# Kernel optimization log

Hardware: AMD Instinct MI355X
Metric: run time of the kernel (lower is better)

The kernel has to match this reference:

```python
import jax, jax.numpy as jnp
import numpy as np

B, T, E, H = 8, 1024, 128, 8
S = E // H  # 16, narrow per-head dim


def setup_inputs() -> dict:
    key = jax.random.key(0)
    ks = jax.random.split(key, 7)
    return {
        "x": jax.random.normal(ks[0], (B, T, E), dtype=jnp.float32),
        "masks": jax.random.randint(ks[1], (B, T), 0, 2, dtype=jnp.int32),
        "Wq": jax.random.normal(ks[2], (S, S), dtype=jnp.float32) * 0.05,
        "Wk": jax.random.normal(ks[3], (S, S), dtype=jnp.float32) * 0.05,
        "Wv": jax.random.normal(ks[4], (S, S), dtype=jnp.float32) * 0.05,
        "Wu": jax.random.normal(ks[5], (E, E), dtype=jnp.float32) * 0.05,
        "bu": jnp.zeros((E,), dtype=jnp.float32),
        "temporal_only": 1,
    }


def reference(x, masks, Wq, Wk, Wv, Wu, bu, temporal_only):
    b, t, e = x.shape
    h = H
    s = e // h
    x4 = x.reshape(b, t, h, s)
    # nn.Linear(s, s, bias=False): y = x @ W.T, applied per head
    q = jnp.einsum('bths,ds->bthd', x4, Wq)
    k = jnp.einsum('bths,ds->bthd', x4, Wk)
    v = jnp.einsum('bths,ds->bthd', x4, Wv)
    scale = jnp.float32(e) ** 0.25
    q = q / scale
    k = k / scale
    # (b, h, t, t) attention logits
    dot = jnp.einsum('bqhd,bkhd->bhqk', q, k)
    # temporal_only masking: masks is (b, t), applied on key axis then query axis
    m = masks.astype(bool)
    neg = jnp.float32(-1e9)
    dot = jnp.where(m[:, None, None, :], dot, neg)
    dot = jnp.where(m[:, None, :, None], dot, neg)
    attn = jax.nn.softmax(dot, axis=-1)
    # post-softmax zeroing with the same masks
    attn = jnp.where(m[:, None, None, :], attn, jnp.float32(0.0))
    attn = jnp.where(m[:, None, :, None], attn, jnp.float32(0.0))
    out = jnp.einsum('bhqk,bkhd->bqhd', attn, v).reshape(b, t, h * s)
    return out @ Wu.T + bu
```

## Files before the change

### kernel.cpp

```cpp
#include <hip/hip_runtime.h>

#define NB 8
#define NT 1024
#define NE 128
#define NH 8
#define NS 16

#define WS_Q 0
#define WS_K 1048576
#define WS_V 2097152
#define WS_Y 3145728
#define WS_VIDX 4194304

#define WT_PITCH 132

static __device__ __forceinline__ void fma4(float4& acc, float s, const float4 v) {
  acc.x = fmaf(s, v.x, acc.x);
  acc.y = fmaf(s, v.y, acc.y);
  acc.z = fmaf(s, v.z, acc.z);
  acc.w = fmaf(s, v.w, acc.w);
}

static __device__ __forceinline__ float dot16(const float4 x0, const float4 x1,
                                              const float4 x2, const float4 x3,
                                              const float4 w0, const float4 w1,
                                              const float4 w2, const float4 w3) {
  float s0 = (x0.x * w0.x + x0.y * w0.y) + (x0.z * w0.z + x0.w * w0.w);
  float s1 = (x1.x * w1.x + x1.y * w1.y) + (x1.z * w1.z + x1.w * w1.w);
  float s2 = (x2.x * w2.x + x2.y * w2.y) + (x2.z * w2.z + x2.w * w2.w);
  float s3 = (x3.x * w3.x + x3.y * w3.y) + (x3.z * w3.z + x3.w * w3.w);
  return (s0 + s1) + (s2 + s3);
}

__global__ __launch_bounds__(256) void qkv_kernel(
    const float* __restrict__ x, const int* __restrict__ masks,
    const float* __restrict__ Wq, const float* __restrict__ Wk,
    const float* __restrict__ Wv, float* __restrict__ Q, float* __restrict__ K,
    float* __restrict__ V, int* __restrict__ vidx, int* __restrict__ vcount) {
  if (blockIdx.x >= 1024) {
    const int b = blockIdx.x - 1024;
    const int lane = threadIdx.x;
    if (lane < 64) {
      int base = 0;
      for (int c = 0; c < NT; c += 64) {
        int t = c + lane;
        int v = masks[b * NT + t] != 0;
        unsigned long long bal = __ballot(v);
        int pos = base + __popcll(bal & ((1ull << lane) - 1ull));
        if (v) vidx[b * NT + pos] = t;
        base += __popcll(bal);
      }
      if (lane == 0) vcount[b] = base;
    }
    return;
  }
  const int tid = threadIdx.x;
  const int h = blockIdx.x & 7;
  const int rg = blockIdx.x >> 3;
  const int b = rg >> 4;
  const int base = rg << 6;
  const int d = tid & 15;
  const int r = base + ((tid >> 4) << 2);
  const float4* wq4 = (const float4*)(Wq + d * 16);
  const float4 wq0 = wq4[0], wq1 = wq4[1], wq2 = wq4[2], wq3 = wq4[3];
  const float4* wk4 = (const float4*)(Wk + d * 16);
  const float4 wk0 = wk4[0], wk1 = wk4[1], wk2 = wk4[2], wk3 = wk4[3];
  const float4* wv4 = (const float4*)(Wv + d * 16);
  const float4 wv0 = wv4[0], wv1 = wv4[1], wv2 = wv4[2], wv3 = wv4[3];
  const float invs = 0.08838834764831845f;
#pragma unroll
  for (int i = 0; i < 4; i++) {
    const int row = r + i;
    const float4* xp = (const float4*)(x + (size_t)row * 128 + h * 16);
    const float4 x0 = xp[0], x1 = xp[1], x2 = xp[2], x3 = xp[3];
    float aq = dot16(x0, x1, x2, x3, wq0, wq1, wq2, wq3);
    float ak = dot16(x0, x1, x2, x3, wk0, wk1, wk2, wk3);
    float av = dot16(x0, x1, x2, x3, wv0, wv1, wv2, wv3);
    const int t = row & 1023;
    size_t o = ((size_t)(b * NH + h) * NT + t) * NS + d;
    Q[o] = aq * invs;
    K[o] = ak;
    V[o] = av;
  }
}

__global__ __launch_bounds__(256) void attn_kernel(
    const float* __restrict__ Q, const float* __restrict__ K,
    const float* __restrict__ V, const int* __restrict__ masks,
    const int* __restrict__ vidx, const int* __restrict__ vcount,
    float* __restrict__ Y) {
  __shared__ __align__(16) float Ks[2048];
  __shared__ __align__(16) float Vs[2048];
  __shared__ __align__(16) float om[2][4][64][20];
  __shared__ float ml[2][4][64][2];
  const int tid = threadIdx.x;
  const int lane = tid & 63;
  const int split = tid >> 6;
  const int bh = blockIdx.x >> 3;
  const int b = bh >> 3, h = bh & 7;
  const int tbase = (blockIdx.x & 7) << 7;
  const int tA = tbase + lane;
  const int nv = vcount[b];
  const float4* qga = (const float4*)(Q + ((size_t)bh * NT + tA) * NS);
  const float4 qa0 = qga[0], qa1 = qga[1], qa2 = qga[2], qa3 = qga[3];
  const float4* qgb = (const float4*)(Q + ((size_t)bh * NT + tA + 64) * NS);
  const float4 qb0 = qgb[0], qb1 = qgb[1], qb2 = qgb[2], qb3 = qgb[3];
  float mA = -1e30f, lA = 0.f, mB = -1e30f, lB = 0.f;
  float4 oa0 = {0, 0, 0, 0}, oa1 = {0, 0, 0, 0}, oa2 = {0, 0, 0, 0},
         oa3 = {0, 0, 0, 0};
  float4 ob0 = {0, 0, 0, 0}, ob1 = {0, 0, 0, 0}, ob2 = {0, 0, 0, 0},
         ob3 = {0, 0, 0, 0};

  for (int k0 = 0; k0 < nv; k0 += 128) {
    __syncthreads();
    const int quad = tid & 3;
    const int jr = tid >> 2;
#pragma unroll
    for (int p = 0; p < 2; p++) {
      int row = jr + (p << 6);
      int j = k0 + row;
      float4 kv = {0, 0, 0, 0}, vv = {0, 0, 0, 0};
      if (j < nv) {
        int kk = vidx[b * NT + j];
        size_t bse = ((size_t)bh * NT + kk) * NS + (quad << 2);
        kv = *(const float4*)(K + bse);
        vv = *(const float4*)(V + bse);
      }
      *(float4*)(Ks + row * 16 + (quad << 2)) = kv;
      *(float4*)(Vs + row * 16 + (quad << 2)) = vv;
    }
    __syncthreads();
    int jmax = nv - k0;
    if (jmax > 128) jmax = 128;
    for (int g = 0; g < 8; g++) {
      const int rbase = split + (g << 4);
      if (rbase >= jmax) break;
      float sA[4], sB[4];
#pragma unroll
      for (int i = 0; i < 4; i++) {
        const float4* kr = (const float4*)(Ks + (rbase + (i << 2)) * 16);
        float4 k0v = kr[0], k1v = kr[1], k2v = kr[2], k3v = kr[3];
        sA[i] = dot16(qa0, qa1, qa2, qa3, k0v, k1v, k2v, k3v);
        sB[i] = dot16(qb0, qb1, qb2, qb3, k0v, k1v, k2v, k3v);
      }
#pragma unroll
      for (int i = 0; i < 4; i++)
        if (rbase + (i << 2) >= jmax) { sA[i] = -1e30f; sB[i] = -1e30f; }
      float mbA = fmaxf(fmaxf(sA[0], sA[1]), fmaxf(sA[2], sA[3]));
      if (mbA > mA) {
        float al = __expf(mA - mbA);
        lA *= al;
        oa0.x *= al; oa0.y *= al; oa0.z *= al; oa0.w *= al;
        oa1.x *= al; oa1.y *= al; oa1.z *= al; oa1.w *= al;
        oa2.x *= al; oa2.y *= al; oa2.z *= al; oa2.w *= al;
        oa3.x *= al; oa3.y *= al; oa3.z *= al; oa3.w *= al;
        mA = mbA;
      }
      float pA[4];
      pA[0] = __expf(sA[0] - mA); pA[1] = __expf(sA[1] - mA);
      pA[2] = __expf(sA[2] - mA); pA[3] = __expf(sA[3] - mA);
      lA += (pA[0] + pA[1]) + (pA[2] + pA[3]);
      float mbB = fmaxf(fmaxf(sB[0], sB[1]), fmaxf(sB[2], sB[3]));
      if (mbB > mB) {
        float al = __expf(mB - mbB);
        lB *= al;
        ob0.x *= al; ob0.y *= al; ob0.z *= al; ob0.w *= al;
        ob1.x *= al; ob1.y *= al; ob1.z *= al; ob1.w *= al;
        ob2.x *= al; ob2.y *= al; ob2.z *= al; ob2.w *= al;
        ob3.x *= al; ob3.y *= al; ob3.z *= al; ob3.w *= al;
        mB = mbB;
      }
      float pB[4];
      pB[0] = __expf(sB[0] - mB); pB[1] = __expf(sB[1] - mB);
      pB[2] = __expf(sB[2] - mB); pB[3] = __expf(sB[3] - mB);
      lB += (pB[0] + pB[1]) + (pB[2] + pB[3]);
#pragma unroll
      for (int i = 0; i < 4; i++) {
        const float4* vr = (const float4*)(Vs + (rbase + (i << 2)) * 16);
        float4 v0 = vr[0], v1 = vr[1], v2 = vr[2], v3 = vr[3];
        fma4(oa0, pA[i], v0); fma4(oa1, pA[i], v1);
        fma4(oa2, pA[i], v2); fma4(oa3, pA[i], v3);
        fma4(ob0, pB[i], v0); fma4(ob1, pB[i], v1);
        fma4(ob2, pB[i], v2); fma4(ob3, pB[i], v3);
      }
    }
  }
  ml[0][split][lane][0] = mA; ml[0][split][lane][1] = lA;
  ml[1][split][lane][0] = mB; ml[1][split][lane][1] = lB;
  {
    float* pa = &om[0][split][lane][0];
    *(float4*)(pa + 0) = oa0; *(float4*)(pa + 4) = oa1;
    *(float4*)(pa + 8) = oa2; *(float4*)(pa + 12) = oa3;
    float* pb = &om[1][split][lane][0];
    *(float4*)(pb + 0) = ob0; *(float4*)(pb + 4) = ob1;
    *(float4*)(pb + 8) = ob2; *(float4*)(pb + 12) = ob3;
  }
  __syncthreads();
  if (split < 2) {
    const int qg = split;
    const int tq = tbase + (qg << 6) + lane;
    float m0 = ml[qg][0][lane][0], l0 = ml[qg][0][lane][1];
    float m1 = ml[qg][1][lane][0], l1 = ml[qg][1][lane][1];
    float m2 = ml[qg][2][lane][0], l2 = ml[qg][2][lane][1];
    float m3 = ml[qg][3][lane][0], l3 = ml[qg][3][lane][1];
    float M = fmaxf(fmaxf(m0, m1), fmaxf(m2, m3));
    float f0 = __expf(m0 - M), f1 = __expf(m1 - M), f2 = __expf(m2 - M),
          f3 = __expf(m3 - M);
    float L = f0 * l0 + f1 * l1 + f2 * l2 + f3 * l3;
    float4 y0 = {0, 0, 0, 0}, y1 = {0, 0, 0, 0}, y2 = {0, 0, 0, 0},
           y3 = {0, 0, 0, 0};
    float fs[4] = {f0, f1, f2, f3};
#pragma unroll
    for (int s = 0; s < 4; s++) {
      const float* p = &om[qg][s][lane][0];
      fma4(y0, fs[s], *(const float4*)(p + 0));
      fma4(y1, fs[s], *(const float4*)(p + 4));
      fma4(y2, fs[s], *(const float4*)(p + 8));
      fma4(y3, fs[s], *(const float4*)(p + 12));
    }
    const int qm = masks[b * NT + tq];
    const float inv = (qm != 0 && L > 0.f) ? (1.0f / L) : 0.f;
    y0.x *= inv; y0.y *= inv; y0.z *= inv; y0.w *= inv;
    y1.x *= inv; y1.y *= inv; y1.z *= inv; y1.w *= inv;
    y2.x *= inv; y2.y *= inv; y2.z *= inv; y2.w *= inv;
    y3.x *= inv; y3.y *= inv; y3.z *= inv; y3.w *= inv;
    float4* yo = (float4*)(Y + ((size_t)b * NT + tq) * NE + h * NS);
    yo[0] = y0; yo[1] = y1; yo[2] = y2; yo[3] = y3;
  }
}

__global__ __launch_bounds__(256) void proj_kernel(
    const float* __restrict__ Y, const float* __restrict__ Wu,
    const float* __restrict__ bu, float* __restrict__ out) {
  __shared__ __align__(16) float Wt[64 * WT_PITCH];
  __shared__ __align__(16) float Yt[16 * 128];
  const int tid = threadIdx.x;
  const int r0 = blockIdx.x * 16;
  const float4* yg = (const float4*)(Y + (size_t)r0 * 128);
  float4* yt4 = (float4*)Yt;
  yt4[tid] = yg[tid];
  yt4[tid + 256] = yg[tid + 256];
  const int c0 = (tid & 31) << 2;
  const int rg = (tid >> 5) & 3;
  const int eh = tid >> 7;
  float4 acc0 = {0, 0, 0, 0}, acc1 = {0, 0, 0, 0}, acc2 = {0, 0, 0, 0},
         acc3 = {0, 0, 0, 0};
  for (int e0 = 0; e0 < 128; e0 += 64) {
    __syncthreads();
#pragma unroll
    for (int p = 0; p < 8; p++) {
      int idx = tid + p * 256;
      int c = idx >> 4;
      int es = (idx & 15) << 2;
      float4 w = *(const float4*)(Wu + c * 128 + e0 + es);
      Wt[(es + 0) * WT_PITCH + c] = w.x;
      Wt[(es + 1) * WT_PITCH + c] = w.y;
      Wt[(es + 2) * WT_PITCH + c] = w.z;
      Wt[(es + 3) * WT_PITCH + c] = w.w;
    }
    __syncthreads();
    const int eb = eh << 5;
    const float* y0 = Yt + (rg * 4 + 0) * 128 + e0 + eb;
    const float* y1 = Yt + (rg * 4 + 1) * 128 + e0 + eb;
    const float* y2 = Yt + (rg * 4 + 2) * 128 + e0 + eb;
    const float* y3 = Yt + (rg * 4 + 3) * 128 + e0 + eb;
#pragma unroll 4
    for (int e = 0; e < 32; e += 4) {
      const float* wb = Wt + (eb + e) * WT_PITCH + c0;
      float4 w0 = *(const float4*)(wb + 0 * WT_PITCH);
      float4 w1 = *(const float4*)(wb + 1 * WT_PITCH);
      float4 w2 = *(const float4*)(wb + 2 * WT_PITCH);
      float4 w3 = *(const float4*)(wb + 3 * WT_PITCH);
      float4 ya = *(const float4*)(y0 + e);
      float4 yb = *(const float4*)(y1 + e);
      float4 yc = *(const float4*)(y2 + e);
      float4 yd = *(const float4*)(y3 + e);
      fma4(acc0, ya.x, w0); fma4(acc0, ya.y, w1); fma4(acc0, ya.z, w2); fma4(acc0, ya.w, w3);
      fma4(acc1, yb.x, w0); fma4(acc1, yb.y, w1); fma4(acc1, yb.z, w2); fma4(acc1, yb.w, w3);
      fma4(acc2, yc.x, w0); fma4(acc2, yc.y, w1); fma4(acc2, yc.z, w2); fma4(acc2, yc.w, w3);
      fma4(acc3, yd.x, w0); fma4(acc3, yd.y, w1); fma4(acc3, yd.z, w2); fma4(acc3, yd.w, w3);
    }
  }
  __syncthreads();
  if (eh == 1) {
    float* p = Wt + (tid & 127) * 20;
    *(float4*)(p + 0) = acc0; *(float4*)(p + 4) = acc1;
    *(float4*)(p + 8) = acc2; *(float4*)(p + 12) = acc3;
  }
  __syncthreads();
  if (eh == 0) {
    const float* p = Wt + tid * 20;
    float4 b4 = *(const float4*)(bu + c0);
    float4 q0 = *(const float4*)(p + 0);
    float4 q1 = *(const float4*)(p + 4);
    float4 q2 = *(const float4*)(p + 8);
    float4 q3 = *(const float4*)(p + 12);
    acc0.x += q0.x + b4.x; acc0.y += q0.y + b4.y; acc0.z += q0.z + b4.z; acc0.w += q0.w + b4.w;
    acc1.x += q1.x + b4.x; acc1.y += q1.y + b4.y; acc1.z += q1.z + b4.z; acc1.w += q1.w + b4.w;
    acc2.x += q2.x + b4.x; acc2.y += q2.y + b4.y; acc2.z += q2.z + b4.z; acc2.w += q2.w + b4.w;
    acc3.x += q3.x + b4.x; acc3.y += q3.y + b4.y; acc3.z += q3.z + b4.z; acc3.w += q3.w + b4.w;
    *(float4*)(out + (size_t)(r0 + rg * 4 + 0) * 128 + c0) = acc0;
    *(float4*)(out + (size_t)(r0 + rg * 4 + 1) * 128 + c0) = acc1;
    *(float4*)(out + (size_t)(r0 + rg * 4 + 2) * 128 + c0) = acc2;
    *(float4*)(out + (size_t)(r0 + rg * 4 + 3) * 128 + c0) = acc3;
  }
}

extern "C" void kernel_launch(void* const* d_in, const int* in_sizes, int n_in,
                              void* d_out, int out_size, void* d_ws,
                              size_t ws_size, hipStream_t stream) {
  const float* x = (const float*)d_in[0];
  const int* masks = (const int*)d_in[1];
  const float* Wq = (const float*)d_in[2];
  const float* Wk = (const float*)d_in[3];
  const float* Wv = (const float*)d_in[4];
  const float* Wu = (const float*)d_in[5];
  const float* bu = (const float*)d_in[6];
  float* out = (float*)d_out;

  float* ws = (float*)d_ws;
  float* Q = ws + WS_Q;
  float* K = ws + WS_K;
  float* V = ws + WS_V;
  float* Y = ws + WS_Y;
  int* vidx = (int*)(ws + WS_VIDX);
  int* vcount = vidx + NB * NT;

  qkv_kernel<<<1024 + NB, 256, 0, stream>>>(x, masks, Wq, Wk, Wv, Q, K, V,
                                            vidx, vcount);
  attn_kernel<<<NB * NH * (NT / 128), 256, 0, stream>>>(Q, K, V, masks, vidx,
                                                        vcount, Y);
  proj_kernel<<<NB * NT / 16, 256, 0, stream>>>(Y, Wu, bu, out);
}
```

Baseline: 140.6 us.

## Restructure attention so each lane handles four queries with 16-way key split

Each block now covers 64 queries instead of 128, which doubles the grid. Each lane holds 4 query rows, so every K/V row read from LDS is reused four times. Keys are split 16 ways within the block (4 lane groups per wave across 4 waves). Partial softmax states are merged first with cross-lane shuffles and then through shared memory. This cuts LDS read traffic per FLOP and adds parallelism, at the cost of higher register pressure (64 accumulator floats plus 64 query floats) and an extra shuffle reduction stage.

```diff
diff --git a/kernel.cpp b/kernel.cpp
--- a/kernel.cpp
+++ b/kernel.cpp
@@ -19,6 +19,19 @@
   acc.y = fmaf(s, v.y, acc.y);
   acc.z = fmaf(s, v.z, acc.z);
   acc.w = fmaf(s, v.w, acc.w);
+}
+
+static __device__ __forceinline__ float dot16f(const float4 q0, const float4 q1,
+                                               const float4 q2, const float4 q3,
+                                               const float4 k0, const float4 k1,
+                                               const float4 k2, const float4 k3) {
+  float s = q0.x * k0.x;
+  s = fmaf(q0.y, k0.y, s); s = fmaf(q0.z, k0.z, s); s = fmaf(q0.w, k0.w, s);
+  s = fmaf(q1.x, k1.x, s); s = fmaf(q1.y, k1.y, s); s = fmaf(q1.z, k1.z, s);
+  s = fmaf(q1.w, k1.w, s); s = fmaf(q2.x, k2.x, s); s = fmaf(q2.y, k2.y, s);
+  s = fmaf(q2.z, k2.z, s); s = fmaf(q2.w, k2.w, s); s = fmaf(q3.x, k3.x, s);
+  s = fmaf(q3.y, k3.y, s); s = fmaf(q3.z, k3.z, s); s = fmaf(q3.w, k3.w, s);
+  return s;
 }
 
 static __device__ __forceinline__ float dot16(const float4 x0, const float4 x1,
@@ -30,6 +43,15 @@
   float s2 = (x2.x * w2.x + x2.y * w2.y) + (x2.z * w2.z + x2.w * w2.w);
   float s3 = (x3.x * w3.x + x3.y * w3.y) + (x3.z * w3.z + x3.w * w3.w);
   return (s0 + s1) + (s2 + s3);
+}
+
+static __device__ __forceinline__ float4 shfl_xor4(const float4 v, int mask) {
+  float4 r;
+  r.x = __shfl_xor(v.x, mask, 64);
+  r.y = __shfl_xor(v.y, mask, 64);
+  r.z = __shfl_xor(v.z, mask, 64);
+  r.w = __shfl_xor(v.w, mask, 64);
+  return r;
 }
 
 __global__ __launch_bounds__(256) void qkv_kernel(
@@ -91,25 +113,33 @@
     float* __restrict__ Y) {
   __shared__ __align__(16) float Ks[2048];
   __shared__ __align__(16) float Vs[2048];
-  __shared__ __align__(16) float om[2][4][64][20];
-  __shared__ float ml[2][4][64][2];
+  __shared__ __align__(16) float om[4][16][4][20];
+  __shared__ float mlw[4][16][4][2];
   const int tid = threadIdx.x;
+  const int wave = tid >> 6;
   const int lane = tid & 63;
-  const int split = tid >> 6;
-  const int bh = blockIdx.x >> 3;
+  const int grp = lane >> 4;
+  const int slot = lane & 15;
+  const int sp = (wave << 2) | grp;
+  const int bh = blockIdx.x >> 4;
   const int b = bh >> 3, h = bh & 7;
-  const int tbase = (blockIdx.x & 7) << 7;
-  const int tA = tbase + lane;
+  const int tbase = (blockIdx.x & 15) << 6;
+  const int tq = tbase + (slot << 2);
   const int nv = vcount[b];
-  const float4* qga = (const float4*)(Q + ((size_t)bh * NT + tA) * NS);
-  const float4 qa0 = qga[0], qa1 = qga[1], qa2 = qga[2], qa3 = qga[3];
-  const float4* qgb = (const float4*)(Q + ((size_t)bh * NT + tA + 64) * NS);
-  const float4 qb0 = qgb[0], qb1 = qgb[1], qb2 = qgb[2], qb3 = qgb[3];
-  float mA = -1e30f, lA = 0.f, mB = -1e30f, lB = 0.f;
-  float4 oa0 = {0, 0, 0, 0}, oa1 = {0, 0, 0, 0}, oa2 = {0, 0, 0, 0},
-         oa3 = {0, 0, 0, 0};
-  float4 ob0 = {0, 0, 0, 0}, ob1 = {0, 0, 0, 0}, ob2 = {0, 0, 0, 0},
-         ob3 = {0, 0, 0, 0};
+  const float4* qg = (const float4*)(Q + ((size_t)bh * NT + tq) * NS);
+  float4 qr[4][4];
+#pragma unroll
+  for (int i = 0; i < 4; i++) {
+#pragma unroll
+    for (int c = 0; c < 4; c++) qr[i][c] = qg[i * 4 + c];
+  }
+  float m[4] = {-1e30f, -1e30f, -1e30f, -1e30f};
+  float l[4] = {0.f, 0.f, 0.f, 0.f};
+  float4 o[4][4];
+#pragma unroll
+  for (int i = 0; i < 4; i++)
+#pragma unroll
+    for (int c = 0; c < 4; c++) o[i][c] = make_float4(0.f, 0.f, 0.f, 0.f);
 
   for (int k0 = 0; k0 < nv; k0 += 128) {
     __syncthreads();
@@ -132,99 +162,134 @@
     __syncthreads();
     int jmax = nv - k0;
     if (jmax > 128) jmax = 128;
-    for (int g = 0; g < 8; g++) {
-      const int rbase = split + (g << 4);
-      if (rbase >= jmax) break;
-      float sA[4], sB[4];
+#pragma unroll
+    for (int g = 0; g < 2; g++) {
+      const int rb = sp + (g << 6);
+      float s[4][4];
 #pragma unroll
       for (int i = 0; i < 4; i++) {
-        const float4* kr = (const float4*)(Ks + (rbase + (i << 2)) * 16);
-        float4 k0v = kr[0], k1v = kr[1], k2v = kr[2], k3v = kr[3];
-        sA[i] = dot16(qa0, qa1, qa2, qa3, k0v, k1v, k2v, k3v);
-        sB[i] = dot16(qb0, qb1, qb2, qb3, k0v, k1v, k2v, k3v);
-      }
-#pragma unroll
-      for (int i = 0; i < 4; i++)
-        if (rbase + (i << 2) >= jmax) { sA[i] = -1e30f; sB[i] = -1e30f; }
-      float mbA = fmaxf(fmaxf(sA[0], sA[1]), fmaxf(sA[2], sA[3]));
-      if (mbA > mA) {
-        float al = __expf(mA - mbA);
-        lA *= al;
-        oa0.x *= al; oa0.y *= al; oa0.z *= al; oa0.w *= al;
-        oa1.x *= al; oa1.y *= al; oa1.z *= al; oa1.w *= al;
-        oa2.x *= al; oa2.y *= al; oa2.z *= al; oa2.w *= al;
-        oa3.x *= al; oa3.y *= al; oa3.z *= al; oa3.w *= al;
-        mA = mbA;
-      }
-      float pA[4];
-      pA[0] = __expf(sA[0] - mA); pA[1] = __expf(sA[1] - mA);
-      pA[2] = __expf(sA[2] - mA); pA[3] = __expf(sA[3] - mA);
-      lA += (pA[0] + pA[1]) + (pA[2] + pA[3]);
-      float mbB = fmaxf(fmaxf(sB[0], sB[1]), fmaxf(sB[2], sB[3]));
-      if (mbB > mB) {
-        float al = __expf(mB - mbB);
-        lB *= al;
-        ob0.x *= al; ob0.y *= al; ob0.z *= al; ob0.w *= al;
-        ob1.x *= al; ob1.y *= al; ob1.z *= al; ob1.w *= al;
-        ob2.x *= al; ob2.y *= al; ob2.z *= al; ob2.w *= al;
-        ob3.x *= al; ob3.y *= al; ob3.z *= al; ob3.w *= al;
-        mB = mbB;
-      }
-      float pB[4];
-      pB[0] = __expf(sB[0] - mB); pB[1] = __expf(sB[1] - mB);
-      pB[2] = __expf(sB[2] - mB); pB[3] = __expf(sB[3] - mB);
-      lB += (pB[0] + pB[1]) + (pB[2] + pB[3]);
+        const float4* kr = (const float4*)(Ks + (rb + (i << 4)) * 16);
+        const float4 k0v = kr[0], k1v = kr[1], k2v = kr[2], k3v = kr[3];
+#pragma unroll
+        for (int q = 0; q < 4; q++)
+          s[i][q] = dot16f(qr[q][0], qr[q][1], qr[q][2], qr[q][3], k0v, k1v,
+                           k2v, k3v);
+      }
 #pragma unroll
       for (int i = 0; i < 4; i++) {
-        const float4* vr = (const float4*)(Vs + (rbase + (i << 2)) * 16);
-        float4 v0 = vr[0], v1 = vr[1], v2 = vr[2], v3 = vr[3];
-        fma4(oa0, pA[i], v0); fma4(oa1, pA[i], v1);
-        fma4(oa2, pA[i], v2); fma4(oa3, pA[i], v3);
-        fma4(ob0, pB[i], v0); fma4(ob1, pB[i], v1);
-        fma4(ob2, pB[i], v2); fma4(ob3, pB[i], v3);
-      }
-    }
-  }
-  ml[0][split][lane][0] = mA; ml[0][split][lane][1] = lA;
-  ml[1][split][lane][0] = mB; ml[1][split][lane][1] = lB;
-  {
-    float* pa = &om[0][split][lane][0];
-    *(float4*)(pa + 0) = oa0; *(float4*)(pa + 4) = oa1;
-    *(float4*)(pa + 8) = oa2; *(float4*)(pa + 12) = oa3;
-    float* pb = &om[1][split][lane][0];
-    *(float4*)(pb + 0) = ob0; *(float4*)(pb + 4) = ob1;
-    *(float4*)(pb + 8) = ob2; *(float4*)(pb + 12) = ob3;
+        if (rb + (i << 4) >= jmax) {
+          s[i][0] = -1e30f; s[i][1] = -1e30f; s[i][2] = -1e30f; s[i][3] = -1e30f;
+        }
+      }
+      float p[4][4];
+#pragma unroll
+      for (int q = 0; q < 4; q++) {
+        float mb = fmaxf(fmaxf(s[0][q], s[1][q]), fmaxf(s[2][q], s[3][q]));
+        if (mb > m[q]) {
+          float al = __expf(m[q] - mb);
+          l[q] *= al;
+#pragma unroll
+          for (int c = 0; c < 4; c++) {
+            o[q][c].x *= al; o[q][c].y *= al; o[q][c].z *= al; o[q][c].w *= al;
+          }
+          m[q] = mb;
+        }
+        p[0][q] = __expf(s[0][q] - m[q]);
+        p[1][q] = __expf(s[1][q] - m[q]);
+        p[2][q] = __expf(s[2][q] - m[q]);
+        p[3][q] = __expf(s[3][q] - m[q]);
+        l[q] += (p[0][q] + p[1][q]) + (p[2][q] + p[3][q]);
+      }
+#pragma unroll
+      for (int i = 0; i < 4; i++) {
+        const float4* vr = (const float4*)(Vs + (rb + (i << 4)) * 16);
+        const float4 v0 = vr[0], v1 = vr[1], v2 = vr[2], v3 = vr[3];
+#pragma unroll
+        for (int q = 0; q < 4; q++) {
+          fma4(o[q][0], p[i][q], v0);
+          fma4(o[q][1], p[i][q], v1);
+          fma4(o[q][2], p[i][q], v2);
+          fma4(o[q][3], p[i][q], v3);
+        }
+      }
+    }
+  }
+#pragma unroll
+  for (int round = 0; round < 2; round++) {
+    const int xm = 16 << round;
+#pragma unroll
+    for (int q = 0; q < 4; q++) {
+      float mo = __shfl_xor(m[q], xm, 64);
+      float lo = __shfl_xor(l[q], xm, 64);
+      float4 oo0 = shfl_xor4(o[q][0], xm);
+      float4 oo1 = shfl_xor4(o[q][1], xm);
+      float4 oo2 = shfl_xor4(o[q][2], xm);
+      float4 oo3 = shfl_xor4(o[q][3], xm);
+      float M2 = fmaxf(m[q], mo);
+      float fs = __expf(m[q] - M2);
+      float fo = __expf(mo - M2);
+      l[q] = fmaf(fs, l[q], fo * lo);
+      o[q][0].x = fmaf(fs, o[q][0].x, fo * oo0.x);
+      o[q][0].y = fmaf(fs, o[q][0].y, fo * oo0.y);
+      o[q][0].z = fmaf(fs, o[q][0].z, fo * oo0.z);
+      o[q][0].w = fmaf(fs, o[q][0].w, fo * oo0.w);
+      o[q][1].x = fmaf(fs, o[q][1].x, fo * oo1.x);
+      o[q][1].y = fmaf(fs, o[q][1].y, fo * oo1.y);
+      o[q][1].z = fmaf(fs, o[q][1].z, fo * oo1.z);
+      o[q][1].w = fmaf(fs, o[q][1].w, fo * oo1.w);
+      o[q][2].x = fmaf(fs, o[q][2].x, fo * oo2.x);
+      o[q][2].y = fmaf(fs, o[q][2].y, fo * oo2.y);
+      o[q][2].z = fmaf(fs, o[q][2].z, fo * oo2.z);
+      o[q][2].w = fmaf(fs, o[q][2].w, fo * oo2.w);
+      o[q][3].x = fmaf(fs, o[q][3].x, fo * oo3.x);
+      o[q][3].y = fmaf(fs, o[q][3].y, fo * oo3.y);
+      o[q][3].z = fmaf(fs, o[q][3].z, fo * oo3.z);
+      o[q][3].w = fmaf(fs, o[q][3].w, fo * oo3.w);
+      m[q] = M2;
+    }
+  }
+  if (grp == 0) {
+#pragma unroll
+    for (int q = 0; q < 4; q++) {
+      float* pp = &om[wave][slot][q][0];
+      *(float4*)(pp + 0) = o[q][0];
+      *(float4*)(pp + 4) = o[q][1];
+      *(float4*)(pp + 8) = o[q][2];
+      *(float4*)(pp + 12) = o[q][3];
+      mlw[wave][slot][q][0] = m[q];
+      mlw[wave][slot][q][1] = l[q];
+    }
   }
   __syncthreads();
-  if (split < 2) {
-    const int qg = split;
-    const int tq = tbase + (qg << 6) + lane;
-    float m0 = ml[qg][0][lane][0], l0 = ml[qg][0][lane][1];
-    float m1 = ml[qg][1][lane][0], l1 = ml[qg][1][lane][1];
-    float m2 = ml[qg][2][lane][0], l2 = ml[qg][2][lane][1];
-    float m3 = ml[qg][3][lane][0], l3 = ml[qg][3][lane][1];
-    float M = fmaxf(fmaxf(m0, m1), fmaxf(m2, m3));
-    float f0 = __expf(m0 - M), f1 = __expf(m1 - M), f2 = __expf(m2 - M),
-          f3 = __expf(m3 - M);
-    float L = f0 * l0 + f1 * l1 + f2 * l2 + f3 * l3;
+  if (wave == 0) {
+    const int fslot = lane >> 2, fq = lane & 3;
+    float mw0 = mlw[0][fslot][fq][0], lw0 = mlw[0][fslot][fq][1];
+    float mw1 = mlw[1][fslot][fq][0], lw1 = mlw[1][fslot][fq][1];
+    float mw2 = mlw[2][fslot][fq][0], lw2 = mlw[2][fslot][fq][1];
+    float mw3 = mlw[3][fslot][fq][0], lw3 = mlw[3][fslot][fq][1];
+    float M = fmaxf(fmaxf(mw0, mw1), fmaxf(mw2, mw3));
+    float f0 = __expf(mw0 - M), f1 = __expf(mw1 - M), f2 = __expf(mw2 - M),
+          f3 = __expf(mw3 - M);
+    float L = f0 * lw0 + f1 * lw1 + f2 * lw2 + f3 * lw3;
+    float fs[4] = {f0, f1, f2, f3};
     float4 y0 = {0, 0, 0, 0}, y1 = {0, 0, 0, 0}, y2 = {0, 0, 0, 0},
            y3 = {0, 0, 0, 0};
-    float fs[4] = {f0, f1, f2, f3};
-#pragma unroll
-    for (int s = 0; s < 4; s++) {
-      const float* p = &om[qg][s][lane][0];
-      fma4(y0, fs[s], *(const float4*)(p + 0));
-      fma4(y1, fs[s], *(const float4*)(p + 4));
-      fma4(y2, fs[s], *(const float4*)(p + 8));
-      fma4(y3, fs[s], *(const float4*)(p + 12));
-    }
-    const int qm = masks[b * NT + tq];
+#pragma unroll
+    for (int w = 0; w < 4; w++) {
+      const float* pp = &om[w][fslot][fq][0];
+      fma4(y0, fs[w], *(const float4*)(pp + 0));
+      fma4(y1, fs[w], *(const float4*)(pp + 4));
+      fma4(y2, fs[w], *(const float4*)(pp + 8));
+      fma4(y3, fs[w], *(const float4*)(pp + 12));
+    }
+    const int tqq = tbase + (fslot << 2) + fq;
+    const int qm = masks[b * NT + tqq];
     const float inv = (qm != 0 && L > 0.f) ? (1.0f / L) : 0.f;
     y0.x *= inv; y0.y *= inv; y0.z *= inv; y0.w *= inv;
     y1.x *= inv; y1.y *= inv; y1.z *= inv; y1.w *= inv;
     y2.x *= inv; y2.y *= inv; y2.z *= inv; y2.w *= inv;
     y3.x *= inv; y3.y *= inv; y3.z *= inv; y3.w *= inv;
-    float4* yo = (float4*)(Y + ((size_t)b * NT + tq) * NE + h * NS);
+    float4* yo = (float4*)(Y + ((size_t)b * NT + tqq) * NE + h * NS);
     yo[0] = y0; yo[1] = y1; yo[2] = y2; yo[3] = y3;
   }
 }
@@ -328,7 +393,7 @@
 
   qkv_kernel<<<1024 + NB, 256, 0, stream>>>(x, masks, Wq, Wk, Wv, Q, K, V,
                                             vidx, vcount);
-  attn_kernel<<<NB * NH * (NT / 128), 256, 0, stream>>>(Q, K, V, masks, vidx,
-                                                        vcount, Y);
+  attn_kernel<<<NB * NH * (NT / 64), 256, 0, stream>>>(Q, K, V, masks, vidx,
+                                                       vcount, Y);
   proj_kernel<<<NB * NT / 16, 256, 0, stream>>>(Y, Wu, bu, out);
 }
```

Measured after the change: 195.2 us. +38.8%, slower.

## Split attention into 64-query blocks with 8-way key split and shuffle merge

Applied to the files above, without the earlier changes.

Each attention block now handles 64 queries instead of 128, so twice as many blocks launch. Within a block the keys are split eight ways (four waves times two half-waves). Each half-wave holds 32 queries times 2. The two half-wave partial softmax states are merged with cross-lane shuffles before the shared-memory merge across waves. The per-tile loop is fully unrolled with masking in place of an early break, and the QK dot uses a serial fma chain. This adds parallelism to fill more CUs, but each block loads K/V tiles for fewer queries, so K/V reuse drops and tile-load traffic rises.

```diff
diff --git a/kernel.cpp b/kernel.cpp
--- a/kernel.cpp
+++ b/kernel.cpp
@@ -19,6 +19,19 @@
   acc.y = fmaf(s, v.y, acc.y);
   acc.z = fmaf(s, v.z, acc.z);
   acc.w = fmaf(s, v.w, acc.w);
+}
+
+static __device__ __forceinline__ float dot16f(const float4 q0, const float4 q1,
+                                               const float4 q2, const float4 q3,
+                                               const float4 k0, const float4 k1,
+                                               const float4 k2, const float4 k3) {
+  float s = q0.x * k0.x;
+  s = fmaf(q0.y, k0.y, s); s = fmaf(q0.z, k0.z, s); s = fmaf(q0.w, k0.w, s);
+  s = fmaf(q1.x, k1.x, s); s = fmaf(q1.y, k1.y, s); s = fmaf(q1.z, k1.z, s);
+  s = fmaf(q1.w, k1.w, s); s = fmaf(q2.x, k2.x, s); s = fmaf(q2.y, k2.y, s);
+  s = fmaf(q2.z, k2.z, s); s = fmaf(q2.w, k2.w, s); s = fmaf(q3.x, k3.x, s);
+  s = fmaf(q3.y, k3.y, s); s = fmaf(q3.z, k3.z, s); s = fmaf(q3.w, k3.w, s);
+  return s;
 }
 
 static __device__ __forceinline__ float dot16(const float4 x0, const float4 x1,
@@ -91,19 +104,21 @@
     float* __restrict__ Y) {
   __shared__ __align__(16) float Ks[2048];
   __shared__ __align__(16) float Vs[2048];
-  __shared__ __align__(16) float om[2][4][64][20];
-  __shared__ float ml[2][4][64][2];
+  __shared__ __align__(16) float om[4][32][2][20];
+  __shared__ float mlw[4][32][2][2];
   const int tid = threadIdx.x;
+  const int wave = tid >> 6;
   const int lane = tid & 63;
-  const int split = tid >> 6;
-  const int bh = blockIdx.x >> 3;
+  const int slot = lane & 31;
+  const int sp = (wave << 1) | (lane >> 5);
+  const int bh = blockIdx.x >> 4;
   const int b = bh >> 3, h = bh & 7;
-  const int tbase = (blockIdx.x & 7) << 7;
-  const int tA = tbase + lane;
+  const int tbase = (blockIdx.x & 15) << 6;
+  const int tA = tbase + slot;
   const int nv = vcount[b];
   const float4* qga = (const float4*)(Q + ((size_t)bh * NT + tA) * NS);
   const float4 qa0 = qga[0], qa1 = qga[1], qa2 = qga[2], qa3 = qga[3];
-  const float4* qgb = (const float4*)(Q + ((size_t)bh * NT + tA + 64) * NS);
+  const float4* qgb = (const float4*)(Q + ((size_t)bh * NT + tA + 32) * NS);
   const float4 qb0 = qgb[0], qb1 = qgb[1], qb2 = qgb[2], qb3 = qgb[3];
   float mA = -1e30f, lA = 0.f, mB = -1e30f, lB = 0.f;
   float4 oa0 = {0, 0, 0, 0}, oa1 = {0, 0, 0, 0}, oa2 = {0, 0, 0, 0},
@@ -132,20 +147,22 @@
     __syncthreads();
     int jmax = nv - k0;
     if (jmax > 128) jmax = 128;
-    for (int g = 0; g < 8; g++) {
-      const int rbase = split + (g << 4);
-      if (rbase >= jmax) break;
+#pragma unroll
+    for (int g = 0; g < 4; g++) {
       float sA[4], sB[4];
 #pragma unroll
       for (int i = 0; i < 4; i++) {
-        const float4* kr = (const float4*)(Ks + (rbase + (i << 2)) * 16);
-        float4 k0v = kr[0], k1v = kr[1], k2v = kr[2], k3v = kr[3];
-        sA[i] = dot16(qa0, qa1, qa2, qa3, k0v, k1v, k2v, k3v);
-        sB[i] = dot16(qb0, qb1, qb2, qb3, k0v, k1v, k2v, k3v);
-      }
-#pragma unroll
-      for (int i = 0; i < 4; i++)
-        if (rbase + (i << 2) >= jmax) { sA[i] = -1e30f; sB[i] = -1e30f; }
+        const int r = sp + (g << 5) + (i << 3);
+        const float4* kr = (const float4*)(Ks + r * 16);
+        const float4 k0v = kr[0], k1v = kr[1], k2v = kr[2], k3v = kr[3];
+        sA[i] = dot16f(qa0, qa1, qa2, qa3, k0v, k1v, k2v, k3v);
+        sB[i] = dot16f(qb0, qb1, qb2, qb3, k0v, k1v, k2v, k3v);
+      }
+#pragma unroll
+      for (int i = 0; i < 4; i++) {
+        const int r = sp + (g << 5) + (i << 3);
+        if (r >= jmax) { sA[i] = -1e30f; sB[i] = -1e30f; }
+      }
       float mbA = fmaxf(fmaxf(sA[0], sA[1]), fmaxf(sA[2], sA[3]));
       if (mbA > mA) {
         float al = __expf(mA - mbA);
@@ -176,8 +193,9 @@
       lB += (pB[0] + pB[1]) + (pB[2] + pB[3]);
 #pragma unroll
       for (int i = 0; i < 4; i++) {
-        const float4* vr = (const float4*)(Vs + (rbase + (i << 2)) * 16);
-        float4 v0 = vr[0], v1 = vr[1], v2 = vr[2], v3 = vr[3];
+        const int r = sp + (g << 5) + (i << 3);
+        const float4* vr = (const float4*)(Vs + r * 16);
+        const float4 v0 = vr[0], v1 = vr[1], v2 = vr[2], v3 = vr[3];
         fma4(oa0, pA[i], v0); fma4(oa1, pA[i], v1);
         fma4(oa2, pA[i], v2); fma4(oa3, pA[i], v3);
         fma4(ob0, pB[i], v0); fma4(ob1, pB[i], v1);
@@ -185,46 +203,72 @@
       }
     }
   }
-  ml[0][split][lane][0] = mA; ml[0][split][lane][1] = lA;
-  ml[1][split][lane][0] = mB; ml[1][split][lane][1] = lB;
   {
-    float* pa = &om[0][split][lane][0];
+    float mo = __shfl_xor(mA, 32, 64);
+    float lo = __shfl_xor(lA, 32, 64);
+    float M2 = fmaxf(mA, mo);
+    float fs = __expf(mA - M2), fo = __expf(mo - M2);
+    lA = fmaf(fs, lA, fo * lo);
+#define MRG(oc)                                                   \
+  {                                                               \
+    float4 t = oc;                                                \
+    t.x = fmaf(fs, oc.x, fo * __shfl_xor(oc.x, 32, 64));          \
+    t.y = fmaf(fs, oc.y, fo * __shfl_xor(oc.y, 32, 64));          \
+    t.z = fmaf(fs, oc.z, fo * __shfl_xor(oc.z, 32, 64));          \
+    t.w = fmaf(fs, oc.w, fo * __shfl_xor(oc.w, 32, 64));          \
+    oc = t;                                                       \
+  }
+    MRG(oa0) MRG(oa1) MRG(oa2) MRG(oa3)
+    mA = M2;
+    mo = __shfl_xor(mB, 32, 64);
+    lo = __shfl_xor(lB, 32, 64);
+    M2 = fmaxf(mB, mo);
+    fs = __expf(mB - M2); fo = __expf(mo - M2);
+    lB = fmaf(fs, lB, fo * lo);
+    MRG(ob0) MRG(ob1) MRG(ob2) MRG(ob3)
+    mB = M2;
+#undef MRG
+  }
+  if (lane < 32) {
+    float* pa = &om[wave][slot][0][0];
     *(float4*)(pa + 0) = oa0; *(float4*)(pa + 4) = oa1;
     *(float4*)(pa + 8) = oa2; *(float4*)(pa + 12) = oa3;
-    float* pb = &om[1][split][lane][0];
+    float* pb = &om[wave][slot][1][0];
     *(float4*)(pb + 0) = ob0; *(float4*)(pb + 4) = ob1;
     *(float4*)(pb + 8) = ob2; *(float4*)(pb + 12) = ob3;
+    mlw[wave][slot][0][0] = mA; mlw[wave][slot][0][1] = lA;
+    mlw[wave][slot][1][0] = mB; mlw[wave][slot][1][1] = lB;
   }
   __syncthreads();
-  if (split < 2) {
-    const int qg = split;
-    const int tq = tbase + (qg << 6) + lane;
-    float m0 = ml[qg][0][lane][0], l0 = ml[qg][0][lane][1];
-    float m1 = ml[qg][1][lane][0], l1 = ml[qg][1][lane][1];
-    float m2 = ml[qg][2][lane][0], l2 = ml[qg][2][lane][1];
-    float m3 = ml[qg][3][lane][0], l3 = ml[qg][3][lane][1];
-    float M = fmaxf(fmaxf(m0, m1), fmaxf(m2, m3));
-    float f0 = __expf(m0 - M), f1 = __expf(m1 - M), f2 = __expf(m2 - M),
-          f3 = __expf(m3 - M);
-    float L = f0 * l0 + f1 * l1 + f2 * l2 + f3 * l3;
+  if (wave == 0) {
+    const int fq = lane >> 5, fslot = lane & 31;
+    float mw0 = mlw[0][fslot][fq][0], lw0 = mlw[0][fslot][fq][1];
+    float mw1 = mlw[1][fslot][fq][0], lw1 = mlw[1][fslot][fq][1];
+    float mw2 = mlw[2][fslot][fq][0], lw2 = mlw[2][fslot][fq][1];
+    float mw3 = mlw[3][fslot][fq][0], lw3 = mlw[3][fslot][fq][1];
+    float M = fmaxf(fmaxf(mw0, mw1), fmaxf(mw2, mw3));
+    float f0 = __expf(mw0 - M), f1 = __expf(mw1 - M), f2 = __expf(mw2 - M),
+          f3 = __expf(mw3 - M);
+    float L = f0 * lw0 + f1 * lw1 + f2 * lw2 + f3 * lw3;
+    float fs[4] = {f0, f1, f2, f3};
     float4 y0 = {0, 0, 0, 0}, y1 = {0, 0, 0, 0}, y2 = {0, 0, 0, 0},
            y3 = {0, 0, 0, 0};
-    float fs[4] = {f0, f1, f2, f3};
-#pragma unroll
-    for (int s = 0; s < 4; s++) {
-      const float* p = &om[qg][s][lane][0];
-      fma4(y0, fs[s], *(const float4*)(p + 0));
-      fma4(y1, fs[s], *(const float4*)(p + 4));
-      fma4(y2, fs[s], *(const float4*)(p + 8));
-      fma4(y3, fs[s], *(const float4*)(p + 12));
-    }
-    const int qm = masks[b * NT + tq];
+#pragma unroll
+    for (int w = 0; w < 4; w++) {
+      const float* pp = &om[w][fslot][fq][0];
+      fma4(y0, fs[w], *(const float4*)(pp + 0));
+      fma4(y1, fs[w], *(const float4*)(pp + 4));
+      fma4(y2, fs[w], *(const float4*)(pp + 8));
+      fma4(y3, fs[w], *(const float4*)(pp + 12));
+    }
+    const int tqq = tbase + lane;
+    const int qm = masks[b * NT + tqq];
     const float inv = (qm != 0 && L > 0.f) ? (1.0f / L) : 0.f;
     y0.x *= inv; y0.y *= inv; y0.z *= inv; y0.w *= inv;
     y1.x *= inv; y1.y *= inv; y1.z *= inv; y1.w *= inv;
     y2.x *= inv; y2.y *= inv; y2.z *= inv; y2.w *= inv;
     y3.x *= inv; y3.y *= inv; y3.z *= inv; y3.w *= inv;
-    float4* yo = (float4*)(Y + ((size_t)b * NT + tq) * NE + h * NS);
+    float4* yo = (float4*)(Y + ((size_t)b * NT + tqq) * NE + h * NS);
     yo[0] = y0; yo[1] = y1; yo[2] = y2; yo[3] = y3;
   }
 }
@@ -328,7 +372,7 @@
 
   qkv_kernel<<<1024 + NB, 256, 0, stream>>>(x, masks, Wq, Wk, Wv, Q, K, V,
                                             vidx, vcount);
-  attn_kernel<<<NB * NH * (NT / 128), 256, 0, stream>>>(Q, K, V, masks, vidx,
-                                                        vcount, Y);
+  attn_kernel<<<NB * NH * (NT / 64), 256, 0, stream>>>(Q, K, V, masks, vidx,
+                                                       vcount, Y);
   proj_kernel<<<NB * NT / 16, 256, 0, stream>>>(Y, Wu, bu, out);
 }
```

Result: slower. 200.2 us (+42.4%).
